# Kernel optimization log

Hardware: AMD Instinct MI355X
Metric: run time of the kernel (lower is better)

The kernel has to match this reference:

```python
import jax, jax.numpy as jnp
import numpy as np

N, E = 50000, 800000
IN_CH, H, OUT_CH, ED, L = 64, 128, 128, 1, 4


def setup_inputs() -> dict:
    key = jax.random.key(0)
    ks = jax.random.split(key, 24)
    s = 0.02
    inp = {
        'h': jax.random.normal(ks[0], (N, IN_CH), jnp.float32),
        'coords': jax.random.normal(ks[1], (N, 3), jnp.float32),
        'edge_attr': jax.random.normal(ks[2], (E, ED), jnp.float32),
        'emb_in_W': jax.random.normal(ks[3], (IN_CH, H), jnp.float32) * s,
        'emb_in_b': jnp.zeros((H,), jnp.float32),
        'emb_out_W': jax.random.normal(ks[4], (H, OUT_CH), jnp.float32) * s,
        'emb_out_b': jnp.zeros((OUT_CH,), jnp.float32),
        # per-layer stacked params
        'eW1': jax.random.normal(ks[5], (L, 2 * H + 1 + ED, H), jnp.float32) * s,
        'eb1': jnp.zeros((L, H), jnp.float32),
        'eW2': jax.random.normal(ks[6], (L, H, H), jnp.float32) * s,
        'eb2': jnp.zeros((L, H), jnp.float32),
        'cW1': jax.random.normal(ks[7], (L, H, H), jnp.float32) * s,
        'cb1': jnp.zeros((L, H), jnp.float32),
        'cWc': jax.random.normal(ks[8], (L, H, 1), jnp.float32) * 0.001,  # xavier gain=0.001, no bias
        'nW1': jax.random.normal(ks[9], (L, 2 * H, H), jnp.float32) * s,
        'nb1': jnp.zeros((L, H), jnp.float32),
        'nW2': jax.random.normal(ks[10], (L, H, H), jnp.float32) * s,
        'nb2': jnp.zeros((L, H), jnp.float32),
        'edge_index': jax.random.randint(ks[11], (2, E), 0, N, jnp.int32),
    }
    return inp


def _egnn_forward(h, coords, edge_attr, emb_in_W, emb_in_b, emb_out_W, emb_out_b,
                  eW1, eb1, eW2, eb2, cW1, cb1, cWc, nW1, nb1, nW2, nb2, edge_index):
    silu = jax.nn.silu
    row, col = edge_index[0], edge_index[1]  # PyG: j=source=row, i=target=col
    # count of incoming edges per target node, for coords_agg='mean'
    counts = jax.ops.segment_sum(jnp.ones((E,), jnp.float32), col, num_segments=N)
    counts = jnp.maximum(counts, 1.0)[:, None]
    h = h @ emb_in_W + emb_in_b
    for l in range(L):
        coord_diff = coords[row] - coords[col]                       # [E,3]
        dist = jnp.sum(coord_diff * coord_diff, axis=-1, keepdims=True)  # [E,1]
        # message: edge MLP on cat(x_i, x_j, dist, edge_attr)
        edge_in = jnp.concatenate([h[col], h[row], dist, edge_attr], axis=-1)
        ef = silu(edge_in @ eW1[l] + eb1[l])
        ef = silu(ef @ eW2[l] + eb2[l])                               # [E,H]
        cw = silu(ef @ cW1[l] + cb1[l]) @ cWc[l]                      # [E,1]
        coord_upd = coord_diff * cw                                   # [E,3]
        # aggregate to target nodes
        agg_feat = jax.ops.segment_sum(ef, col, num_segments=N)       # [N,H]
        agg_coord = jax.ops.segment_sum(coord_upd, col, num_segments=N) / counts
        # node update (residual)
        node_in = jnp.concatenate([h, agg_feat], axis=-1)
        upd = silu(node_in @ nW1[l] + nb1[l]) @ nW2[l] + nb2[l]
        h = h + upd
        coords = coords + agg_coord
    h = h @ emb_out_W + emb_out_b
    return h, coords


def reference(h, coords, edge_attr, emb_in_W, emb_in_b, emb_out_W, emb_out_b,
              eW1, eb1, eW2, eb2, cW1, cb1, cWc, nW1, nb1, nW2, nb2, edge_index):
    return _egnn_forward(h, coords, edge_attr, emb_in_W, emb_in_b, emb_out_W, emb_out_b,
                         eW1, eb1, eW2, eb2, cW1, cb1, cWc, nW1, nb1, nW2, nb2, edge_index)
```

## Files before the change

### kernel.cpp

```cpp
#include <hip/hip_runtime.h>

constexpr int Nn = 50000;
constexpr int Ee = 800000;
constexpr int EF_STR  = 136;
constexpr int NIN_STR = 264;
constexpr int HIN_STR = 72;
constexpr int NB_SCAN = (Nn + 255) / 256;

typedef short s8v __attribute__((ext_vector_type(8)));
typedef float f4v __attribute__((ext_vector_type(4)));

__device__ __forceinline__ ushort f2bf(float f) {
    uint u = __float_as_uint(f);
    uint r = (u + 0x7FFFu + ((u >> 16) & 1u)) >> 16;
    return (ushort)r;
}
__device__ __forceinline__ ushort f2bf_t(float f) {
    return (ushort)(__float_as_uint(f) >> 16);
}
__device__ __forceinline__ float bf2f(ushort s) {
    return __uint_as_float(((uint)s) << 16);
}
__device__ __forceinline__ float silu_f(float x) {
    return x * __fdividef(1.0f, 1.0f + __expf(-x));
}
__device__ __forceinline__ uint pack2bf_t(float lo, float hi) {
    return __builtin_amdgcn_perm(__float_as_uint(hi), __float_as_uint(lo), 0x07060302u);
}
__device__ __forceinline__ uint pack2bf_r(float lo, float hi) {
    uint a = __float_as_uint(lo) + 0x8000u;
    uint b = __float_as_uint(hi) + 0x8000u;
    return __builtin_amdgcn_perm(b, a, 0x07060302u);
}

__device__ __forceinline__ void swz_one(const float* src, ushort* dst, int K, int lstride, int KC, int idx)
{
    int per = KC * 4096;
    int l = idx / per, r = idx % per;
    int fb = r >> 9, rem = r & 511;
    int lane = rem >> 3, jj = rem & 7;
    int kc = fb >> 3, t = fb & 7;
    int k = kc * 32 + ((lane >> 4) << 3) + jj;
    int n = t * 16 + (lane & 15);
    float v = (k < K) ? src[(size_t)l * lstride + (size_t)k * 128 + n] : 0.0f;
    dst[idx] = f2bf(v);
}
__global__ void __launch_bounds__(256) k_swz_all(
    const float* __restrict__ eW1, const float* __restrict__ eW2, const float* __restrict__ cW1,
    const float* __restrict__ nW1, const float* __restrict__ nW2,
    const float* __restrict__ inW, const float* __restrict__ outW,
    ushort* __restrict__ oT, ushort* __restrict__ oM,
    ushort* __restrict__ o2, ushort* __restrict__ o3,
    ushort* __restrict__ o4, ushort* __restrict__ o5,
    ushort* __restrict__ o6, ushort* __restrict__ o7)
{
    int gid = blockIdx.x * 256 + threadIdx.x;
    if (gid < 65536)       swz_one(eW1,         oT, 128, 33024, 4, gid);
    else if (gid < 131072) swz_one(eW1 + 16384, oM, 128, 33024, 4, gid - 65536);
    else if (gid < 196608) swz_one(eW2, o2, 128, 16384, 4, gid - 131072);
    else if (gid < 262144) swz_one(cW1, o3, 128, 16384, 4, gid - 196608);
    else if (gid < 393216) swz_one(nW1, o4, 256, 32768, 8, gid - 262144);
    else if (gid < 458752) swz_one(nW2, o5, 128, 16384, 4, gid - 393216);
    else if (gid < 466944) swz_one(inW, o6, 64, 8192, 2, gid - 458752);
    else if (gid < 483328) swz_one(outW, o7, 128, 16384, 4, gid - 466944);
}

__global__ void __launch_bounds__(256) k_count(const int* __restrict__ eidx, int* __restrict__ ecnt)
{
    int e = blockIdx.x * 256 + threadIdx.x;
    atomicAdd(&ecnt[eidx[Ee + e]], 1);
}

__global__ void __launch_bounds__(256) k_bsum(const int* __restrict__ ecnt, int* __restrict__ bsum)
{
    __shared__ int ws[4];
    int tid = threadIdx.x, lane = tid & 63, w = tid >> 6;
    int i = blockIdx.x * 256 + tid;
    int x = (i < Nn) ? ecnt[i] : 0;
    #pragma unroll
    for (int off = 1; off < 64; off <<= 1) x += __shfl_xor(x, off, 64);
    if (lane == 0) ws[w] = x;
    __syncthreads();
    if (tid == 0) bsum[blockIdx.x] = ws[0] + ws[1] + ws[2] + ws[3];
}
__global__ void __launch_bounds__(256) k_bscan(int* __restrict__ bsum)
{
    __shared__ int ws[4];
    int tid = threadIdx.x, lane = tid & 63, w = tid >> 6;
    int x = (tid < NB_SCAN) ? bsum[tid] : 0;
    int s = x;
    #pragma unroll
    for (int off = 1; off < 64; off <<= 1) {
        int t = __shfl_up(s, off, 64);
        if (lane >= off) s += t;
    }
    if (lane == 63) ws[w] = s;
    __syncthreads();
    if (tid == 0) { int a = 0; for (int k = 0; k < 4; k++) { int t = ws[k]; ws[k] = a; a += t; } }
    __syncthreads();
    int excl = ws[w] + s - x;
    if (tid < NB_SCAN) bsum[tid] = excl;
}
__global__ void __launch_bounds__(256) k_cursor(const int* __restrict__ ecnt,
                                               const int* __restrict__ boff, int* __restrict__ cursor)
{
    __shared__ int ws[4];
    int tid = threadIdx.x, lane = tid & 63, w = tid >> 6;
    int i = blockIdx.x * 256 + tid;
    int x = (i < Nn) ? ecnt[i] : 0;
    int s = x;
    #pragma unroll
    for (int off = 1; off < 64; off <<= 1) {
        int t = __shfl_up(s, off, 64);
        if (lane >= off) s += t;
    }
    if (lane == 63) ws[w] = s;
    __syncthreads();
    if (tid == 0) { int a = 0; for (int k = 0; k < 4; k++) { int t = ws[k]; ws[k] = a; a += t; } }
    __syncthreads();
    int excl = ws[w] + s - x + boff[blockIdx.x];
    if (i < Nn) cursor[i] = excl;
}

__global__ void __launch_bounds__(256) k_scatter(
    const int* __restrict__ eidx, const float* __restrict__ edge_attr,
    int* __restrict__ cursor,
    int* __restrict__ srow, int* __restrict__ scol, float* __restrict__ sattr)
{
    int e = blockIdx.x * 256 + threadIdx.x;
    int r = eidx[e], c = eidx[Ee + e];
    int p = atomicAdd(&cursor[c], 1);
    srow[p] = r; scol[p] = c; sattr[p] = edge_attr[e];
}

__global__ void __launch_bounds__(512, 2) k_emb(
    const float* __restrict__ h_in, const float* __restrict__ coords,
    const ushort* __restrict__ ws_, const float* __restrict__ b,
    float* __restrict__ hbuf, ushort* __restrict__ hbf, float* __restrict__ cbuf,
    const ushort* __restrict__ topW, const ushort* __restrict__ midW,
    const float* __restrict__ b1, ushort* __restrict__ uvb)
{
    __shared__ alignas(16) ushort s_h[64 * HIN_STR];
    __shared__ alignas(16) ushort s_hb[64 * EF_STR];
    const int tid = threadIdx.x;
    const int nb = blockIdx.x * 64;
    #pragma unroll
    for (int i = 0; i < 2; i++) {
        int idx = i * 512 + tid;
        int e = idx >> 4, ch = idx & 15;
        int node = nb + e;
        float4 f = make_float4(0.f, 0.f, 0.f, 0.f);
        if (node < Nn) f = *(const float4*)(h_in + (size_t)node * 64 + ch * 4);
        ushort4 u; u.x = f2bf(f.x); u.y = f2bf(f.y); u.z = f2bf(f.z); u.w = f2bf(f.w);
        *(ushort4*)(s_h + e * HIN_STR + ch * 4) = u;
    }
    if (tid < 192) {
        int n = nb + tid / 3, d = tid % 3;
        if (n < Nn) cbuf[n * 3 + d] = coords[n * 3 + d];
    }
    __syncthreads();
    const int lane = tid & 63, wave = tid >> 6;
    const int m = lane & 15, quad = lane >> 4;
    const int ws2 = wave >> 2, wt = wave & 3;
    const int rbase = ws2 * 32;
    {
        f4v acc[2][2];
        #pragma unroll
        for (int nt = 0; nt < 2; nt++) { acc[nt][0] = (f4v){0,0,0,0}; acc[nt][1] = (f4v){0,0,0,0}; }
        const ushort* aBase = ws_ + wt * 1024 + lane * 8;
        #pragma unroll
        for (int kc = 0; kc < 2; kc++) {
            s8v a0 = *(const s8v*)(aBase + kc * 4096);
            s8v a1 = *(const s8v*)(aBase + kc * 4096 + 512);
            #pragma unroll
            for (int nt = 0; nt < 2; nt++) {
                s8v bf = *(const s8v*)(s_h + (rbase + nt * 16 + m) * HIN_STR + kc * 32 + quad * 8);
                acc[nt][0] = __builtin_amdgcn_mfma_f32_16x16x32_bf16(a0, bf, acc[nt][0], 0, 0, 0);
                acc[nt][1] = __builtin_amdgcn_mfma_f32_16x16x32_bf16(a1, bf, acc[nt][1], 0, 0, 0);
            }
        }
        #pragma unroll
        for (int nt = 0; nt < 2; nt++) {
            int node = nb + rbase + nt * 16 + m;
            #pragma unroll
            for (int ct = 0; ct < 2; ct++) {
                int colb = (wt * 2 + ct) * 16 + quad * 4;
                uint2 pk = make_uint2(0u, 0u);
                if (node < Nn) {
                    float4 bb = *(const float4*)(b + colb);
                    float v0 = acc[nt][ct][0] + bb.x;
                    float v1 = acc[nt][ct][1] + bb.y;
                    float v2 = acc[nt][ct][2] + bb.z;
                    float v3 = acc[nt][ct][3] + bb.w;
                    *(float4*)(hbuf + (size_t)node * 128 + colb) = make_float4(v0, v1, v2, v3);
                    pk.x = pack2bf_r(v0, v1); pk.y = pack2bf_r(v2, v3);
                    *(uint2*)(hbf + (size_t)node * 128 + colb) = pk;
                }
                *(uint2*)(s_hb + (rbase + nt * 16 + m) * EF_STR + colb) = pk;
            }
        }
    }
    __syncthreads();
    {
        f4v au[2][2], av[2][2];
        #pragma unroll
        for (int ct = 0; ct < 2; ct++) {
            float4 bb = *(const float4*)(b1 + (wt * 2 + ct) * 16 + quad * 4);
            au[0][ct] = (f4v){bb.x, bb.y, bb.z, bb.w};
            au[1][ct] = au[0][ct];
            av[0][ct] = (f4v){0,0,0,0};
            av[1][ct] = (f4v){0,0,0,0};
        }
        const ushort* tBase = topW + wt * 1024 + (size_t)lane * 8;
        const ushort* mBase = midW + wt * 1024 + (size_t)lane * 8;
        #pragma unroll
        for (int kc = 0; kc < 4; kc++) {
            s8v t0 = *(const s8v*)(tBase + kc * 4096);
            s8v t1 = *(const s8v*)(tBase + kc * 4096 + 512);
            s8v m0 = *(const s8v*)(mBase + kc * 4096);
            s8v m1 = *(const s8v*)(mBase + kc * 4096 + 512);
            #pragma unroll
            for (int nt = 0; nt < 2; nt++) {
                s8v bf = *(const s8v*)(s_hb + (rbase + nt * 16 + m) * EF_STR + kc * 32 + quad * 8);
                au[nt][0] = __builtin_amdgcn_mfma_f32_16x16x32_bf16(t0, bf, au[nt][0], 0, 0, 0);
                au[nt][1] = __builtin_amdgcn_mfma_f32_16x16x32_bf16(t1, bf, au[nt][1], 0, 0, 0);
                av[nt][0] = __builtin_amdgcn_mfma_f32_16x16x32_bf16(m0, bf, av[nt][0], 0, 0, 0);
                av[nt][1] = __builtin_amdgcn_mfma_f32_16x16x32_bf16(m1, bf, av[nt][1], 0, 0, 0);
            }
        }
        #pragma unroll
        for (int nt = 0; nt < 2; nt++) {
            int node = nb + rbase + nt * 16 + m;
            if (node < Nn) {
                #pragma unroll
                for (int ct = 0; ct < 2; ct++) {
                    int colb = (wt * 2 + ct) * 16 + quad * 4;
                    uint2 pu; pu.x = pack2bf_r(au[nt][ct][0], au[nt][ct][1]);
                              pu.y = pack2bf_r(au[nt][ct][2], au[nt][ct][3]);
                    *(uint2*)(uvb + (size_t)node * 256 + colb) = pu;
                    uint2 pv; pv.x = pack2bf_r(av[nt][ct][0], av[nt][ct][1]);
                              pv.y = pack2bf_r(av[nt][ct][2], av[nt][ct][3]);
                    *(uint2*)(uvb + (size_t)node * 256 + 128 + colb) = pv;
                }
            }
        }
    }
}

__device__ __forceinline__ uint uv_term(uint uw, uint vw, float dist, float attr,
                                        const float* wdp, const float* wap, int j)
{
    float2 w2d = *(const float2*)(wdp + 2 * j);
    float2 w2a = *(const float2*)(wap + 2 * j);
    float lo = __uint_as_float(uw << 16) + __uint_as_float(vw << 16)
             + dist * w2d.x + attr * w2a.x;
    float hi = __uint_as_float(uw & 0xFFFF0000u) + __uint_as_float(vw & 0xFFFF0000u)
             + dist * w2d.y + attr * w2a.y;
    return pack2bf_t(silu_f(lo), silu_f(hi));
}

__global__ void __launch_bounds__(512, 8) k_edge(
    const float* __restrict__ cbuf,
    const int* __restrict__ srow, const int* __restrict__ scol, const float* __restrict__ sattr,
    const ushort* __restrict__ uvb,
    const float* __restrict__ wd, const float* __restrict__ wa,
    const ushort* __restrict__ w2s, const float* __restrict__ b2,
    const ushort* __restrict__ cw1s, const float* __restrict__ cb1,
    const float* __restrict__ cwc,
    float* __restrict__ agg_feat, float* __restrict__ agg_coord)
{
    __shared__ alignas(16) ushort s_a[128 * EF_STR];
    __shared__ alignas(16) float  s_p[128 * 4];
    __shared__ float s_dist[128];
    __shared__ int   s_col[128];
    __shared__ float s_cd[128 * 3];
    __shared__ alignas(16) float s_wd[128];
    __shared__ alignas(16) float s_wa[128];

    const int tid = threadIdx.x;
    const int eb = blockIdx.x * 128;

    if (tid < 128) {
        int rw = srow[eb + tid], cl = scol[eb + tid];
        s_col[tid] = cl;
        float d0 = cbuf[rw * 3 + 0] - cbuf[cl * 3 + 0];
        float d1 = cbuf[rw * 3 + 1] - cbuf[cl * 3 + 1];
        float d2 = cbuf[rw * 3 + 2] - cbuf[cl * 3 + 2];
        s_cd[tid * 3 + 0] = d0; s_cd[tid * 3 + 1] = d1; s_cd[tid * 3 + 2] = d2;
        s_dist[tid] = d0 * d0 + d1 * d1 + d2 * d2;
    } else if (tid < 256) {
        s_wd[tid - 128] = wd[tid - 128];
    } else if (tid < 384) {
        s_wa[tid - 256] = wa[tid - 256];
    }
    __syncthreads();

    {
        const int e = tid >> 2, ch = tid & 3;
        int row = srow[eb + e], col = scol[eb + e];
        float attr = sattr[eb + e];
        float dist = s_dist[e];
        const ushort* up = uvb + (size_t)col * 256 + ch * 32;
        const ushort* vp = uvb + (size_t)row * 256 + 128 + ch * 32;
        #pragma unroll
        for (int hf = 0; hf < 2; hf++) {
            uint4 ua = *(const uint4*)(up + hf * 16);
            uint4 ub = *(const uint4*)(up + hf * 16 + 8);
            uint4 va = *(const uint4*)(vp + hf * 16);
            uint4 vb = *(const uint4*)(vp + hf * 16 + 8);
            const float* wdp = s_wd + ch * 32 + hf * 16;
            const float* wap = s_wa + ch * 32 + hf * 16;
            uint4 q0, q1;
            q0.x = uv_term(ua.x, va.x, dist, attr, wdp, wap, 0);
            q0.y = uv_term(ua.y, va.y, dist, attr, wdp, wap, 1);
            q0.z = uv_term(ua.z, va.z, dist, attr, wdp, wap, 2);
            q0.w = uv_term(ua.w, va.w, dist, attr, wdp, wap, 3);
            *(uint4*)(s_a + e * EF_STR + ch * 32 + hf * 16) = q0;
            q1.x = uv_term(ub.x, vb.x, dist, attr, wdp, wap, 4);
            q1.y = uv_term(ub.y, vb.y, dist, attr, wdp, wap, 5);
            q1.z = uv_term(ub.z, vb.z, dist, attr, wdp, wap, 6);
            q1.w = uv_term(ub.w, vb.w, dist, attr, wdp, wap, 7);
            *(uint4*)(s_a + e * EF_STR + ch * 32 + hf * 16 + 8) = q1;
        }
    }
    __syncthreads();

    const int lane = tid & 63, wave = tid >> 6;
    const int m = lane & 15, quad = lane >> 4;
    const int ws2 = wave >> 2, wt = wave & 3;
    const int rbase = ws2 * 64;

    f4v acc2[4][2];
    {
        #pragma unroll
        for (int tt = 0; tt < 2; tt++) {
            float4 bb = *(const float4*)(b2 + (wt * 2 + tt) * 16 + quad * 4);
            f4v b4 = (f4v){bb.x, bb.y, bb.z, bb.w};
            #pragma unroll
            for (int mt = 0; mt < 4; mt++) acc2[mt][tt] = b4;
        }
        const ushort* bBase = w2s + wt * 1024 + (size_t)lane * 8;
        __builtin_amdgcn_s_setprio(1);
        #pragma unroll
        for (int kc = 0; kc < 4; kc++) {
            s8v b0 = *(const s8v*)(bBase + kc * 4096);
            s8v b1v = *(const s8v*)(bBase + kc * 4096 + 512);
            #pragma unroll
            for (int mt = 0; mt < 4; mt++) {
                s8v a = *(const s8v*)(s_a + (rbase + mt * 16 + m) * EF_STR + kc * 32 + quad * 8);
                acc2[mt][0] = __builtin_amdgcn_mfma_f32_16x16x32_bf16(b0, a, acc2[mt][0], 0, 0, 0);
                acc2[mt][1] = __builtin_amdgcn_mfma_f32_16x16x32_bf16(b1v, a, acc2[mt][1], 0, 0, 0);
            }
        }
        __builtin_amdgcn_s_setprio(0);
    }
    __syncthreads();
    #pragma unroll
    for (int mt = 0; mt < 4; mt++)
        #pragma unroll
        for (int tt = 0; tt < 2; tt++) {
            uint2 pk;
            pk.x = pack2bf_t(silu_f(acc2[mt][tt][0]), silu_f(acc2[mt][tt][1]));
            pk.y = pack2bf_t(silu_f(acc2[mt][tt][2]), silu_f(acc2[mt][tt][3]));
            *(uint2*)(s_a + (rbase + mt * 16 + m) * EF_STR + (wt * 2 + tt) * 16 + quad * 4) = pk;
        }
    __syncthreads();

    {
        f4v acc3[4][2];
        #pragma unroll
        for (int tt = 0; tt < 2; tt++) {
            float4 bb = *(const float4*)(cb1 + (wt * 2 + tt) * 16 + quad * 4);
            f4v b4 = (f4v){bb.x, bb.y, bb.z, bb.w};
            #pragma unroll
            for (int mt = 0; mt < 4; mt++) acc3[mt][tt] = b4;
        }
        const ushort* bBase = cw1s + wt * 1024 + (size_t)lane * 8;
        __builtin_amdgcn_s_setprio(1);
        #pragma unroll
        for (int kc = 0; kc < 4; kc++) {
            s8v b0 = *(const s8v*)(bBase + kc * 4096);
            s8v b1v = *(const s8v*)(bBase + kc * 4096 + 512);
            #pragma unroll
            for (int mt = 0; mt < 4; mt++) {
                s8v a = *(const s8v*)(s_a + (rbase + mt * 16 + m) * EF_STR + kc * 32 + quad * 8);
                acc3[mt][0] = __builtin_amdgcn_mfma_f32_16x16x32_bf16(b0, a, acc3[mt][0], 0, 0, 0);
                acc3[mt][1] = __builtin_amdgcn_mfma_f32_16x16x32_bf16(b1v, a, acc3[mt][1], 0, 0, 0);
            }
        }
        __builtin_amdgcn_s_setprio(0);
        float4 wc0 = *(const float4*)(cwc + (wt * 2 + 0) * 16 + quad * 4);
        float4 wc1 = *(const float4*)(cwc + (wt * 2 + 1) * 16 + quad * 4);
        #pragma unroll
        for (int mt = 0; mt < 4; mt++) {
            float p = silu_f(acc3[mt][0][0]) * wc0.x + silu_f(acc3[mt][0][1]) * wc0.y
                    + silu_f(acc3[mt][0][2]) * wc0.z + silu_f(acc3[mt][0][3]) * wc0.w
                    + silu_f(acc3[mt][1][0]) * wc1.x + silu_f(acc3[mt][1][1]) * wc1.y
                    + silu_f(acc3[mt][1][2]) * wc1.z + silu_f(acc3[mt][1][3]) * wc1.w;
            p += __shfl_xor(p, 16, 64);
            p += __shfl_xor(p, 32, 64);
            if (quad == 0) s_p[(rbase + mt * 16 + m) * 4 + wt] = p;
        }
    }
    __syncthreads();

    if (tid < 128) {
        float4 pt = *(const float4*)(s_p + tid * 4);
        float cw = pt.x + pt.y + pt.z + pt.w;
        int cn = s_col[tid];
        unsafeAtomicAdd(&agg_coord[cn * 3 + 0], s_cd[tid * 3 + 0] * cw);
        unsafeAtomicAdd(&agg_coord[cn * 3 + 1], s_cd[tid * 3 + 1] * cw);
        unsafeAtomicAdd(&agg_coord[cn * 3 + 2], s_cd[tid * 3 + 2] * cw);
    }
    {
        int j = tid & 127;
        int e0 = (tid >> 7) * 32;
        float accv = 0.0f; int cur = s_col[e0];
        #pragma unroll 4
        for (int ee = e0; ee < e0 + 32; ee++) {
            int c = s_col[ee];
            if (c != cur) {
                unsafeAtomicAdd(&agg_feat[(size_t)cur * 128 + j], accv);
                accv = 0.0f; cur = c;
            }
            accv += bf2f(s_a[ee * EF_STR + j]);
        }
        unsafeAtomicAdd(&agg_feat[(size_t)cur * 128 + j], accv);
    }
}

__global__ void __launch_bounds__(512, 6) k_node(
    float* __restrict__ hbuf, ushort* __restrict__ hbf, float* __restrict__ cbuf,
    float* __restrict__ agg_feat, float* __restrict__ agg_coord,
    const int* __restrict__ ecnt,
    const ushort* __restrict__ w1s, const float* __restrict__ b1,
    const ushort* __restrict__ w2s, const float* __restrict__ b2,
    const ushort* __restrict__ topW, const ushort* __restrict__ midW,
    const float* __restrict__ b1e, ushort* __restrict__ uvb, int do_uv)
{
    __shared__ alignas(16) ushort s_nin[64 * NIN_STR];
    __shared__ alignas(16) ushort s_t1[64 * EF_STR];
    const int tid = threadIdx.x;
    const int nb = blockIdx.x * 64;

    #pragma unroll
    for (int i = 0; i < 2; i++) {
        int idx = i * 512 + tid;
        int e = idx >> 4, ch = idx & 15;
        int node = nb + e;
        uint4 v = make_uint4(0, 0, 0, 0);
        if (node < Nn) v = *(const uint4*)(hbf + (size_t)node * 128 + ch * 8);
        *(uint4*)(s_nin + e * NIN_STR + ch * 8) = v;
    }
    #pragma unroll
    for (int i = 0; i < 4; i++) {
        int idx = i * 512 + tid;
        int e = idx >> 5, ch = idx & 31;
        int node = nb + e;
        float4 f = make_float4(0.f, 0.f, 0.f, 0.f);
        if (node < Nn) {
            f = *(const float4*)(agg_feat + (size_t)node * 128 + ch * 4);
            *(float4*)(agg_feat + (size_t)node * 128 + ch * 4) = make_float4(0.f, 0.f, 0.f, 0.f);
        }
        uint2 pk; pk.x = pack2bf_t(f.x, f.y); pk.y = pack2bf_t(f.z, f.w);
        *(uint2*)(s_nin + e * NIN_STR + 128 + ch * 4) = pk;
    }
    if (tid < 64) {
        int n = nb + tid;
        if (n < Nn) {
            float c = (float)ecnt[n]; c = (c < 1.0f) ? 1.0f : c;
            float inv = __fdividef(1.0f, c);
            cbuf[n * 3 + 0] += agg_coord[n * 3 + 0] * inv;
            cbuf[n * 3 + 1] += agg_coord[n * 3 + 1] * inv;
            cbuf[n * 3 + 2] += agg_coord[n * 3 + 2] * inv;
            agg_coord[n * 3 + 0] = 0.f; agg_coord[n * 3 + 1] = 0.f; agg_coord[n * 3 + 2] = 0.f;
        }
    }
    __syncthreads();

    const int lane = tid & 63, wave = tid >> 6;
    const int m = lane & 15, quad = lane >> 4;
    const int ws2 = wave >> 2, wt = wave & 3;
    const int rbase = ws2 * 32;

    {
        f4v acc[2][2];
        #pragma unroll
        for (int ct = 0; ct < 2; ct++) {
            float4 bb = *(const float4*)(b1 + (wt * 2 + ct) * 16 + quad * 4);
            acc[0][ct] = (f4v){bb.x, bb.y, bb.z, bb.w};
            acc[1][ct] = acc[0][ct];
        }
        const ushort* aBase = w1s + wt * 1024 + (size_t)lane * 8;
        #pragma unroll
        for (int kc = 0; kc < 8; kc++) {
            s8v a0 = *(const s8v*)(aBase + kc * 4096);
            s8v a1 = *(const s8v*)(aBase + kc * 4096 + 512);
            #pragma unroll
            for (int nt = 0; nt < 2; nt++) {
                s8v bf = *(const s8v*)(s_nin + (rbase + nt * 16 + m) * NIN_STR + kc * 32 + quad * 8);
                acc[nt][0] = __builtin_amdgcn_mfma_f32_16x16x32_bf16(a0, bf, acc[nt][0], 0, 0, 0);
                acc[nt][1] = __builtin_amdgcn_mfma_f32_16x16x32_bf16(a1, bf, acc[nt][1], 0, 0, 0);
            }
        }
        #pragma unroll
        for (int nt = 0; nt < 2; nt++) {
            int row = rbase + nt * 16 + m;
            #pragma unroll
            for (int ct = 0; ct < 2; ct++) {
                int colb = (wt * 2 + ct) * 16 + quad * 4;
                float v0 = silu_f(acc[nt][ct][0]);
                float v1 = silu_f(acc[nt][ct][1]);
                float v2 = silu_f(acc[nt][ct][2]);
                float v3 = silu_f(acc[nt][ct][3]);
                uint2 pk; pk.x = pack2bf_t(v0, v1); pk.y = pack2bf_t(v2, v3);
                *(uint2*)(s_t1 + row * EF_STR + colb) = pk;
            }
        }
    }
    __syncthreads();

    {
        f4v acc[2][2];
        #pragma unroll
        for (int ct = 0; ct < 2; ct++) {
            float4 bb = *(const float4*)(b2 + (wt * 2 + ct) * 16 + quad * 4);
            acc[0][ct] = (f4v){bb.x, bb.y, bb.z, bb.w};
            acc[1][ct] = acc[0][ct];
        }
        const ushort* aBase = w2s + wt * 1024 + (size_t)lane * 8;
        #pragma unroll
        for (int kc = 0; kc < 4; kc++) {
            s8v a0 = *(const s8v*)(aBase + kc * 4096);
            s8v a1 = *(const s8v*)(aBase + kc * 4096 + 512);
            #pragma unroll
            for (int nt = 0; nt < 2; nt++) {
                s8v bf = *(const s8v*)(s_t1 + (rbase + nt * 16 + m) * EF_STR + kc * 32 + quad * 8);
                acc[nt][0] = __builtin_amdgcn_mfma_f32_16x16x32_bf16(a0, bf, acc[nt][0], 0, 0, 0);
                acc[nt][1] = __builtin_amdgcn_mfma_f32_16x16x32_bf16(a1, bf, acc[nt][1], 0, 0, 0);
            }
        }
        #pragma unroll
        for (int nt = 0; nt < 2; nt++) {
            int node = nb + rbase + nt * 16 + m;
            #pragma unroll
            for (int ct = 0; ct < 2; ct++) {
                int colb = (wt * 2 + ct) * 16 + quad * 4;
                uint2 pk = make_uint2(0u, 0u);
                if (node < Nn) {
                    float4 old = *(const float4*)(hbuf + (size_t)node * 128 + colb);
                    float v0 = old.x + acc[nt][ct][0];
                    float v1 = old.y + acc[nt][ct][1];
                    float v2 = old.z + acc[nt][ct][2];
                    float v3 = old.w + acc[nt][ct][3];
                    *(float4*)(hbuf + (size_t)node * 128 + colb) = make_float4(v0, v1, v2, v3);
                    pk.x = pack2bf_r(v0, v1); pk.y = pack2bf_r(v2, v3);
                    *(uint2*)(hbf + (size_t)node * 128 + colb) = pk;
                }
                if (do_uv)
                    *(uint2*)(s_nin + (rbase + nt * 16 + m) * EF_STR + colb) = pk;
            }
        }
    }

    if (do_uv) {
        __syncthreads();
        f4v au[2][2], av[2][2];
        #pragma unroll
        for (int ct = 0; ct < 2; ct++) {
            float4 bb = *(const float4*)(b1e + (wt * 2 + ct) * 16 + quad * 4);
            au[0][ct] = (f4v){bb.x, bb.y, bb.z, bb.w};
            au[1][ct] = au[0][ct];
            av[0][ct] = (f4v){0,0,0,0};
            av[1][ct] = (f4v){0,0,0,0};
        }
        const ushort* tBase = topW + wt * 1024 + (size_t)lane * 8;
        const ushort* mBase = midW + wt * 1024 + (size_t)lane * 8;
        #pragma unroll
        for (int kc = 0; kc < 4; kc++) {
            s8v t0 = *(const s8v*)(tBase + kc * 4096);
            s8v t1 = *(const s8v*)(tBase + kc * 4096 + 512);
            s8v m0 = *(const s8v*)(mBase + kc * 4096);
            s8v m1 = *(const s8v*)(mBase + kc * 4096 + 512);
            #pragma unroll
            for (int nt = 0; nt < 2; nt++) {
                s8v bf = *(const s8v*)(s_nin + (rbase + nt * 16 + m) * EF_STR + kc * 32 + quad * 8);
                au[nt][0] = __builtin_amdgcn_mfma_f32_16x16x32_bf16(t0, bf, au[nt][0], 0, 0, 0);
                au[nt][1] = __builtin_amdgcn_mfma_f32_16x16x32_bf16(t1, bf, au[nt][1], 0, 0, 0);
                av[nt][0] = __builtin_amdgcn_mfma_f32_16x16x32_bf16(m0, bf, av[nt][0], 0, 0, 0);
                av[nt][1] = __builtin_amdgcn_mfma_f32_16x16x32_bf16(m1, bf, av[nt][1], 0, 0, 0);
            }
        }
        #pragma unroll
        for (int nt = 0; nt < 2; nt++) {
            int node = nb + rbase + nt * 16 + m;
            if (node < Nn) {
                #pragma unroll
                for (int ct = 0; ct < 2; ct++) {
                    int colb = (wt * 2 + ct) * 16 + quad * 4;
                    uint2 pu; pu.x = pack2bf_r(au[nt][ct][0], au[nt][ct][1]);
                              pu.y = pack2bf_r(au[nt][ct][2], au[nt][ct][3]);
                    *(uint2*)(uvb + (size_t)node * 256 + colb) = pu;
                    uint2 pv; pv.x = pack2bf_r(av[nt][ct][0], av[nt][ct][1]);
                              pv.y = pack2bf_r(av[nt][ct][2], av[nt][ct][3]);
                    *(uint2*)(uvb + (size_t)node * 256 + 128 + colb) = pv;
                }
            }
        }
    }
}

__global__ void __launch_bounds__(512, 2) k_emb_out(
    const ushort* __restrict__ hbf, const float* __restrict__ cbuf,
    const ushort* __restrict__ ws_, const float* __restrict__ b, float* __restrict__ out)
{
    __shared__ alignas(16) ushort s_h[64 * EF_STR];
    const int tid = threadIdx.x;
    const int nb = blockIdx.x * 64;
    #pragma unroll
    for (int i = 0; i < 2; i++) {
        int idx = i * 512 + tid;
        int e = idx >> 4, ch = idx & 15;
        int node = nb + e;
        uint4 v = make_uint4(0, 0, 0, 0);
        if (node < Nn) v = *(const uint4*)(hbf + (size_t)node * 128 + ch * 8);
        *(uint4*)(s_h + e * EF_STR + ch * 8) = v;
    }
    if (tid < 192) {
        int n = nb + tid / 3, d = tid % 3;
        if (n < Nn) out[(size_t)Nn * 128 + n * 3 + d] = cbuf[n * 3 + d];
    }
    __syncthreads();
    const int lane = tid & 63, wave = tid >> 6;
    const int m = lane & 15, quad = lane >> 4;
    const int ws2 = wave >> 2, wt = wave & 3;
    const int rbase = ws2 * 32;
    f4v acc[2][2];
    #pragma unroll
    for (int ct = 0; ct < 2; ct++) {
        float4 bb = *(const float4*)(b + (wt * 2 + ct) * 16 + quad * 4);
        acc[0][ct] = (f4v){bb.x, bb.y, bb.z, bb.w};
        acc[1][ct] = acc[0][ct];
    }
    const ushort* aBase = ws_ + wt * 1024 + (size_t)lane * 8;
    #pragma unroll
    for (int kc = 0; kc < 4; kc++) {
        s8v a0 = *(const s8v*)(aBase + kc * 4096);
        s8v a1 = *(const s8v*)(aBase + kc * 4096 + 512);
        #pragma unroll
        for (int nt = 0; nt < 2; nt++) {
            s8v bf = *(const s8v*)(s_h + (rbase + nt * 16 + m) * EF_STR + kc * 32 + quad * 8);
            acc[nt][0] = __builtin_amdgcn_mfma_f32_16x16x32_bf16(a0, bf, acc[nt][0], 0, 0, 0);
            acc[nt][1] = __builtin_amdgcn_mfma_f32_16x16x32_bf16(a1, bf, acc[nt][1], 0, 0, 0);
        }
    }
    #pragma unroll
    for (int nt = 0; nt < 2; nt++) {
        int node = nb + rbase + nt * 16 + m;
        if (node < Nn) {
            #pragma unroll
            for (int ct = 0; ct < 2; ct++) {
                int colb = (wt * 2 + ct) * 16 + quad * 4;
                float4 o = make_float4(acc[nt][ct][0], acc[nt][ct][1],
                                       acc[nt][ct][2], acc[nt][ct][3]);
                *(float4*)(out + (size_t)node * 128 + colb) = o;
            }
        }
    }
}

extern "C" void kernel_launch(void* const* d_in, const int* in_sizes, int n_in,
                              void* d_out, int out_size, void* d_ws, size_t ws_size,
                              hipStream_t stream)
{
    const float* h_in      = (const float*)d_in[0];
    const float* coords    = (const float*)d_in[1];
    const float* edge_attr = (const float*)d_in[2];
    const float* emb_in_W  = (const float*)d_in[3];
    const float* emb_in_b  = (const float*)d_in[4];
    const float* emb_out_W = (const float*)d_in[5];
    const float* emb_out_b = (const float*)d_in[6];
    const float* eW1 = (const float*)d_in[7];
    const float* eb1 = (const float*)d_in[8];
    const float* eW2 = (const float*)d_in[9];
    const float* eb2 = (const float*)d_in[10];
    const float* cW1 = (const float*)d_in[11];
    const float* cb1 = (const float*)d_in[12];
    const float* cWc = (const float*)d_in[13];
    const float* nW1 = (const float*)d_in[14];
    const float* nb1 = (const float*)d_in[15];
    const float* nW2 = (const float*)d_in[16];
    const float* nb2 = (const float*)d_in[17];
    const int*  eidx = (const int*)d_in[18];

    size_t off = 0;
    char* base = (char*)d_ws;
    auto alloc = [&](size_t bytes) -> char* {
        char* p = base + off;
        off += (bytes + 255) & ~(size_t)255;
        return p;
    };
    float*  hbuf      = (float*)alloc((size_t)Nn * 128 * 4);
    ushort* hbf       = (ushort*)alloc((size_t)Nn * 128 * 2);
    ushort* uvb       = (ushort*)alloc((size_t)Nn * 256 * 2);
    float*  cbuf      = (float*)alloc((size_t)Nn * 3 * 4);
    int*    ecnt      = (int*)alloc((size_t)Nn * 4);
    int*    cursor    = (int*)alloc((size_t)Nn * 4);
    int*    bsum      = (int*)alloc((size_t)NB_SCAN * 4);
    int*    srow      = (int*)alloc((size_t)Ee * 4);
    int*    scol      = (int*)alloc((size_t)Ee * 4);
    float*  sattr     = (float*)alloc((size_t)Ee * 4);
    float*  agg_feat  = (float*)alloc((size_t)Nn * 128 * 4);
    float*  agg_coord = (float*)alloc((size_t)Nn * 3 * 4);
    ushort* eW1tops   = (ushort*)alloc((size_t)4 * 16384 * 2);
    ushort* eW1mids   = (ushort*)alloc((size_t)4 * 16384 * 2);
    ushort* eW2s      = (ushort*)alloc((size_t)4 * 16384 * 2);
    ushort* cW1s      = (ushort*)alloc((size_t)4 * 16384 * 2);
    ushort* nW1s      = (ushort*)alloc((size_t)4 * 32768 * 2);
    ushort* nW2s      = (ushort*)alloc((size_t)4 * 16384 * 2);
    ushort* eInWs     = (ushort*)alloc((size_t)8192 * 2);
    ushort* eOutWs    = (ushort*)alloc((size_t)16384 * 2);

    k_swz_all<<<483328 / 256, 256, 0, stream>>>(
        eW1, eW2, cW1, nW1, nW2, emb_in_W, emb_out_W,
        eW1tops, eW1mids, eW2s, cW1s, nW1s, nW2s, eInWs, eOutWs);

    hipMemsetAsync(ecnt, 0, (size_t)Nn * 4, stream);
    k_count<<<Ee / 256, 256, 0, stream>>>(eidx, ecnt);
    k_bsum<<<NB_SCAN, 256, 0, stream>>>(ecnt, bsum);
    k_bscan<<<1, 256, 0, stream>>>(bsum);
    k_cursor<<<NB_SCAN, 256, 0, stream>>>(ecnt, bsum, cursor);
    k_scatter<<<Ee / 256, 256, 0, stream>>>(eidx, edge_attr, cursor, srow, scol, sattr);
    k_emb<<<(Nn + 63) / 64, 512, 0, stream>>>(
        h_in, coords, eInWs, emb_in_b, hbuf, hbf, cbuf,
        eW1tops, eW1mids, eb1, uvb);

    hipMemsetAsync(agg_feat, 0, (size_t)Nn * 128 * 4, stream);
    hipMemsetAsync(agg_coord, 0, (size_t)Nn * 3 * 4, stream);

    for (int l = 0; l < 4; l++) {
        k_edge<<<Ee / 128, 512, 0, stream>>>(
            cbuf, srow, scol, sattr, uvb,
            eW1 + ((size_t)l * 258 + 256) * 128,
            eW1 + ((size_t)l * 258 + 257) * 128,
            eW2s + (size_t)l * 16384, eb2 + l * 128,
            cW1s + (size_t)l * 16384, cb1 + l * 128,
            cWc + l * 128,
            agg_feat, agg_coord);
        int ln = (l < 3) ? (l + 1) : 0;
        k_node<<<(Nn + 63) / 64, 512, 0, stream>>>(
            hbuf, hbf, cbuf, agg_feat, agg_coord, ecnt,
            nW1s + (size_t)l * 32768, nb1 + l * 128,
            nW2s + (size_t)l * 16384, nb2 + l * 128,
            eW1tops + (size_t)ln * 16384, eW1mids + (size_t)ln * 16384,
            eb1 + ln * 128, uvb, (l < 3) ? 1 : 0);
    }
    k_emb_out<<<(Nn + 63) / 64, 512, 0, stream>>>(hbf, cbuf, eOutWs, emb_out_b, (float*)d_out);
}
```

Measured before the change: 1.431 ms.

## Merge edge prologue phases, pack row/col indices, and prefetch W2 fragments

Packs the sorted row and col indices into one int2 array, so the edge kernel reads both with a single load. The separate prologue that staged distances and the wd/wa weights in shared memory is removed, which drops one block-wide barrier: each thread now computes coordinate differences itself, and the weights are read straight from global memory. The first two k-chunks of the W2 MFMA fragments are loaded before the remaining barrier to hide their latency. In exchange, the gather of coords is repeated four times per edge, the weights are read from global memory with redundant loads, and register pressure rises under the 8-waves occupancy bound.

After: 1.728 ms. +20.7%, slower.

```diff
diff --git a/kernel.cpp b/kernel.cpp
--- a/kernel.cpp
+++ b/kernel.cpp
@@ -125,12 +125,12 @@
 __global__ void __launch_bounds__(256) k_scatter(
     const int* __restrict__ eidx, const float* __restrict__ edge_attr,
     int* __restrict__ cursor,
-    int* __restrict__ srow, int* __restrict__ scol, float* __restrict__ sattr)
+    int2* __restrict__ spair, float* __restrict__ sattr)
 {
     int e = blockIdx.x * 256 + threadIdx.x;
     int r = eidx[e], c = eidx[Ee + e];
     int p = atomicAdd(&cursor[c], 1);
-    srow[p] = r; scol[p] = c; sattr[p] = edge_attr[e];
+    spair[p] = make_int2(r, c); sattr[p] = edge_attr[e];
 }
 
 __global__ void __launch_bounds__(512, 2) k_emb(
@@ -261,7 +261,7 @@
 
 __global__ void __launch_bounds__(512, 8) k_edge(
     const float* __restrict__ cbuf,
-    const int* __restrict__ srow, const int* __restrict__ scol, const float* __restrict__ sattr,
+    const int2* __restrict__ spair, const float* __restrict__ sattr,
     const ushort* __restrict__ uvb,
     const float* __restrict__ wd, const float* __restrict__ wa,
     const ushort* __restrict__ w2s, const float* __restrict__ b2,
@@ -271,45 +271,38 @@
 {
     __shared__ alignas(16) ushort s_a[128 * EF_STR];
     __shared__ alignas(16) float  s_p[128 * 4];
-    __shared__ float s_dist[128];
     __shared__ int   s_col[128];
     __shared__ float s_cd[128 * 3];
-    __shared__ alignas(16) float s_wd[128];
-    __shared__ alignas(16) float s_wa[128];
 
     const int tid = threadIdx.x;
     const int eb = blockIdx.x * 128;
-
-    if (tid < 128) {
-        int rw = srow[eb + tid], cl = scol[eb + tid];
-        s_col[tid] = cl;
-        float d0 = cbuf[rw * 3 + 0] - cbuf[cl * 3 + 0];
-        float d1 = cbuf[rw * 3 + 1] - cbuf[cl * 3 + 1];
-        float d2 = cbuf[rw * 3 + 2] - cbuf[cl * 3 + 2];
-        s_cd[tid * 3 + 0] = d0; s_cd[tid * 3 + 1] = d1; s_cd[tid * 3 + 2] = d2;
-        s_dist[tid] = d0 * d0 + d1 * d1 + d2 * d2;
-    } else if (tid < 256) {
-        s_wd[tid - 128] = wd[tid - 128];
-    } else if (tid < 384) {
-        s_wa[tid - 256] = wa[tid - 256];
-    }
-    __syncthreads();
+    const int lane = tid & 63, wave = tid >> 6;
+    const int m = lane & 15, quad = lane >> 4;
+    const int ws2 = wave >> 2, wt = wave & 3;
+    const int rbase = ws2 * 64;
 
     {
         const int e = tid >> 2, ch = tid & 3;
-        int row = srow[eb + e], col = scol[eb + e];
+        int2 rc = spair[eb + e];
         float attr = sattr[eb + e];
-        float dist = s_dist[e];
-        const ushort* up = uvb + (size_t)col * 256 + ch * 32;
-        const ushort* vp = uvb + (size_t)row * 256 + 128 + ch * 32;
+        const ushort* up = uvb + (size_t)rc.y * 256 + ch * 32;
+        const ushort* vp = uvb + (size_t)rc.x * 256 + 128 + ch * 32;
+        float d0 = cbuf[rc.x * 3 + 0] - cbuf[rc.y * 3 + 0];
+        float d1 = cbuf[rc.x * 3 + 1] - cbuf[rc.y * 3 + 1];
+        float d2 = cbuf[rc.x * 3 + 2] - cbuf[rc.y * 3 + 2];
+        float dist = d0 * d0 + d1 * d1 + d2 * d2;
+        if (ch == 0) {
+            s_col[e] = rc.y;
+            s_cd[e * 3 + 0] = d0; s_cd[e * 3 + 1] = d1; s_cd[e * 3 + 2] = d2;
+        }
         #pragma unroll
         for (int hf = 0; hf < 2; hf++) {
             uint4 ua = *(const uint4*)(up + hf * 16);
             uint4 ub = *(const uint4*)(up + hf * 16 + 8);
             uint4 va = *(const uint4*)(vp + hf * 16);
             uint4 vb = *(const uint4*)(vp + hf * 16 + 8);
-            const float* wdp = s_wd + ch * 32 + hf * 16;
-            const float* wap = s_wa + ch * 32 + hf * 16;
+            const float* wdp = wd + ch * 32 + hf * 16;
+            const float* wap = wa + ch * 32 + hf * 16;
             uint4 q0, q1;
             q0.x = uv_term(ua.x, va.x, dist, attr, wdp, wap, 0);
             q0.y = uv_term(ua.y, va.y, dist, attr, wdp, wap, 1);
@@ -323,12 +316,12 @@
             *(uint4*)(s_a + e * EF_STR + ch * 32 + hf * 16 + 8) = q1;
         }
     }
-    __syncthreads();
-
-    const int lane = tid & 63, wave = tid >> 6;
-    const int m = lane & 15, quad = lane >> 4;
-    const int ws2 = wave >> 2, wt = wave & 3;
-    const int rbase = ws2 * 64;
+    const ushort* bBase2 = w2s + wt * 1024 + (size_t)lane * 8;
+    s8v w2f0 = *(const s8v*)(bBase2);
+    s8v w2f1 = *(const s8v*)(bBase2 + 512);
+    s8v w2f2 = *(const s8v*)(bBase2 + 4096);
+    s8v w2f3 = *(const s8v*)(bBase2 + 4096 + 512);
+    __syncthreads();
 
     f4v acc2[4][2];
     {
@@ -339,12 +332,16 @@
             #pragma unroll
             for (int mt = 0; mt < 4; mt++) acc2[mt][tt] = b4;
         }
-        const ushort* bBase = w2s + wt * 1024 + (size_t)lane * 8;
         __builtin_amdgcn_s_setprio(1);
         #pragma unroll
         for (int kc = 0; kc < 4; kc++) {
-            s8v b0 = *(const s8v*)(bBase + kc * 4096);
-            s8v b1v = *(const s8v*)(bBase + kc * 4096 + 512);
+            s8v b0, b1v;
+            if (kc == 0)      { b0 = w2f0; b1v = w2f1; }
+            else if (kc == 1) { b0 = w2f2; b1v = w2f3; }
+            else {
+                b0  = *(const s8v*)(bBase2 + kc * 4096);
+                b1v = *(const s8v*)(bBase2 + kc * 4096 + 512);
+            }
             #pragma unroll
             for (int mt = 0; mt < 4; mt++) {
                 s8v a = *(const s8v*)(s_a + (rbase + mt * 16 + m) * EF_STR + kc * 32 + quad * 8);
@@ -707,8 +704,7 @@
     int*    ecnt      = (int*)alloc((size_t)Nn * 4);
     int*    cursor    = (int*)alloc((size_t)Nn * 4);
     int*    bsum      = (int*)alloc((size_t)NB_SCAN * 4);
-    int*    srow      = (int*)alloc((size_t)Ee * 4);
-    int*    scol      = (int*)alloc((size_t)Ee * 4);
+    int2*   spair     = (int2*)alloc((size_t)Ee * 8);
     float*  sattr     = (float*)alloc((size_t)Ee * 4);
     float*  agg_feat  = (float*)alloc((size_t)Nn * 128 * 4);
     float*  agg_coord = (float*)alloc((size_t)Nn * 3 * 4);
@@ -730,7 +726,7 @@
     k_bsum<<<NB_SCAN, 256, 0, stream>>>(ecnt, bsum);
     k_bscan<<<1, 256, 0, stream>>>(bsum);
     k_cursor<<<NB_SCAN, 256, 0, stream>>>(ecnt, bsum, cursor);
-    k_scatter<<<Ee / 256, 256, 0, stream>>>(eidx, edge_attr, cursor, srow, scol, sattr);
+    k_scatter<<<Ee / 256, 256, 0, stream>>>(eidx, edge_attr, cursor, spair, sattr);
     k_emb<<<(Nn + 63) / 64, 512, 0, stream>>>(
         h_in, coords, eInWs, emb_in_b, hbuf, hbf, cbuf,
         eW1tops, eW1mids, eb1, uvb);
@@ -740,7 +736,7 @@
 
     for (int l = 0; l < 4; l++) {
         k_edge<<<Ee / 128, 512, 0, stream>>>(
-            cbuf, srow, scol, sattr, uvb,
+            cbuf, spair, sattr, uvb,
             eW1 + ((size_t)l * 258 + 256) * 128,
             eW1 + ((size_t)l * 258 + 257) * 128,
             eW2s + (size_t)l * 16384, eb2 + l * 128,
```
